# Performance work log

Measured on AMD Instinct MI355X. Metric: run time of the kernel, lower is better.

Reference implementation:

```python
import jax, jax.numpy as jnp
import numpy as np

B, T, N, H = 256, 64, 128, 128  # batch, seq_len, num_tasks, hidden_dim


def setup_inputs() -> dict:
    key = jax.random.key(0)
    k = jax.random.split(key, 8)
    task_seq = jax.random.randint(k[0], (B, T), 0, N)
    status_seq = jax.random.randint(k[1], (B, T), 0, 3)
    raw = (jax.random.uniform(k[2], (N, N)) < 0.05).astype(jnp.float32)
    adj = raw + jnp.eye(N, dtype=jnp.float32)
    rs = adj.sum(axis=1, keepdims=True)
    adj = adj / jnp.where(rs == 0, 1.0, rs)
    s = np.float32(1.0 / np.sqrt(H))
    emb = jax.random.normal(k[3], (N * 3, H), jnp.float32) * s      # interaction_emb
    W_ih = jax.random.normal(k[4], (3 * H, 2 * H), jnp.float32) * s  # GRUCell weight_ih (r,z,n)
    W_hh = jax.random.normal(k[5], (3 * H, H), jnp.float32) * s      # GRUCell weight_hh
    b_ih = jnp.zeros((3 * H,), jnp.float32)
    b_hh = jnp.zeros((3 * H,), jnp.float32)
    w_pred = jax.random.normal(k[6], (H,), jnp.float32) * s          # predict_layer weight [1,H] -> [H]
    b_pred = jnp.zeros((), jnp.float32)                              # predict_layer bias
    return dict(task_seq=task_seq, status_seq=status_seq, adj=adj, emb=emb,
                W_ih=W_ih, W_hh=W_hh, b_ih=b_ih, b_hh=b_hh,
                w_pred=w_pred, b_pred=b_pred)


def _gru_cell(x, h, W_ih, W_hh, b_ih, b_hh):
    # torch.nn.GRUCell: gates ordered (reset, update, new)
    gi = x @ W_ih.T + b_ih
    gh = h @ W_hh.T + b_hh
    i_r, i_z, i_n = jnp.split(gi, 3, axis=-1)
    h_r, h_z, h_n = jnp.split(gh, 3, axis=-1)
    r = jax.nn.sigmoid(i_r + h_r)
    z = jax.nn.sigmoid(i_z + h_z)
    n = jnp.tanh(i_n + r * h_n)
    return (1.0 - z) * n + z * h


def reference(task_seq, status_seq, adj, emb, W_ih, W_hh, b_ih, b_hh, w_pred, b_pred):
    Bsz, _ = task_seq.shape
    Nt = adj.shape[0]
    Hd = emb.shape[1]
    b_idx = jnp.arange(Bsz)
    h0 = jnp.zeros((Bsz, Nt, Hd), emb.dtype)

    def step(h, ts):
        task, status = ts                                # [B], [B]
        x = emb[task * 3 + status]                       # [B,H] interaction embedding
        # original: full (adj @ h)[b, task]; identical math computing only needed row
        agg = jnp.einsum('bn,bnh->bh', adj[task], h)     # [B,H]
        prev = h[b_idx, task]                            # [B,H]
        new = _gru_cell(jnp.concatenate([x, agg], axis=1), prev, W_ih, W_hh, b_ih, b_hh)
        h = h.at[b_idx, task].set(new)                   # scatter updated target state
        logits = h @ w_pred + b_pred                     # [B,N] predict over all tasks
        return h, logits

    h_final, logits = jax.lax.scan(step, h0, (task_seq.T, status_seq.T))
    return jnp.transpose(logits, (1, 0, 2)), h_final     # ([B,T,N], [B,N,H])
```

## Files before the change

### kernel.cpp

```cpp
#include <hip/hip_runtime.h>

#define B_ 256
#define T_ 64
#define N_ 128
#define H_ 128
#define G3 384
#define K2 256

#define WS_G    0
#define WS_PW   (WS_G + G3*G3)
#define WS_NZC  (WS_PW + K2*G3)
#define WS_NZP  (WS_NZC + 128)

__global__ void __launch_bounds__(384) prep(
        const float* __restrict__ W_ih, const float* __restrict__ W_hh,
        const float* __restrict__ emb,  const float* __restrict__ b_ih,
        const float* __restrict__ adj,  float* __restrict__ ws) {
    const int bid = blockIdx.x;
    if (bid < 384) {
        __shared__ float es[H_];
        const int e = bid, j = threadIdx.x;
        if (j < H_) es[j] = emb[e * H_ + j];
        __syncthreads();
        float acc = b_ih[j];
        const float4* wrow = (const float4*)(W_ih + j * K2);
        #pragma unroll 8
        for (int i = 0; i < 32; ++i) {
            float4 w = wrow[i];
            acc += w.x * es[4*i];
            acc += w.y * es[4*i + 1];
            acc += w.z * es[4*i + 2];
            acc += w.w * es[4*i + 3];
        }
        (ws + WS_G)[e * G3 + j] = acc;
    } else if (bid < 512) {
        __shared__ float row[N_];
        const int r = bid - 384;
        if (threadIdx.x < N_) row[threadIdx.x] = adj[r * N_ + threadIdx.x];
        __syncthreads();
        if (threadIdx.x == 0) {
            int*  nzc = (int*)(ws + WS_NZC);
            int2* nzp = (int2*)(ws + WS_NZP);
            int cnt = 0;
            for (int n = 0; n < N_; ++n) {
                float w = row[n];
                if (w != 0.0f) { nzp[r * N_ + cnt] = make_int2(n, __float_as_int(w)); ++cnt; }
            }
            int cnt4 = (cnt + 3) & ~3;
            for (int i = cnt; i < cnt4; ++i) nzp[r * N_ + i] = make_int2(0, 0);
            nzc[r] = cnt;
        }
    } else {
        const int k = bid - 512, j = threadIdx.x;
        (ws + WS_PW)[k * G3 + j] = (k < H_) ? W_ih[j * K2 + H_ + k]
                                            : W_hh[j * H_ + (k - H_)];
    }
}

__global__ void __launch_bounds__(512, 2) gkt_main(
        const int* __restrict__ task_seq, const int* __restrict__ status_seq,
        const float* __restrict__ b_hh,   const float* __restrict__ w_pred,
        const float* __restrict__ b_pred, const float* __restrict__ ws,
        float* __restrict__ out) {
    __shared__ __align__(16) float h_lds[N_ * H_];
    __shared__ __align__(16) float aggbuf[H_];
    __shared__ float pl[4 * G3];
    __shared__ float red[H_];
    __shared__ float Ll[N_];
    __shared__ int2  nzbuf[N_];
    __shared__ int   nz_cnt;
    __shared__ int   tasks_l[T_], stats_l[T_];

    const int b   = blockIdx.x;
    const int tid = threadIdx.x;
    const int t   = tid & 127;
    const int q   = tid >> 7;

    const float* G   = ws + WS_G;
    const float* PW  = ws + WS_PW;
    const int*   nzc = (const int*)(ws + WS_NZC);
    const int2*  nzp = (const int2*)(ws + WS_NZP);

    float wr[64], wz[64], wn[64];
    {
        const float* base = PW + (q * 64) * G3 + t;
        #pragma unroll
        for (int kk = 0; kk < 64; ++kk) {
            wr[kk] = base[kk * G3];
            wz[kk] = base[kk * G3 + 128];
            wn[kk] = base[kk * G3 + 256];
        }
    }
    const float bp = b_pred[0];
    float bhr = 0.f, bhz = 0.f, bhn = 0.f, wpt = 0.f;
    if (q < 2) { bhr = b_hh[t]; bhz = b_hh[128 + t]; bhn = b_hh[256 + t]; }
    if (q == 0) wpt = w_pred[t];

    for (int i = tid; i < N_ * H_; i += 512) h_lds[i] = 0.0f;
    if (tid < T_)            tasks_l[tid]       = task_seq[b * T_ + tid];
    else if (tid < 2 * T_)   stats_l[tid - T_]  = status_seq[b * T_ + (tid - T_)];
    if (tid < N_) { Ll[tid] = bp; aggbuf[tid] = 0.0f; }
    __syncthreads();

    for (int s = 0; s < T_; ++s) {
        const int task = tasks_l[s];

        float prevreg = 0.f;
        if (q < 2) prevreg = h_lds[task * H_ + t];
        {
            const float* vbase = (q < 2) ? (aggbuf + q * 64)
                                         : (h_lds + task * H_ + (q - 2) * 64);
            float pr = 0.f, pz = 0.f, pn = 0.f;
            #pragma unroll
            for (int kk = 0; kk < 64; kk += 4) {
                const float4 v = *(const float4*)(vbase + kk);
                pr += wr[kk] * v.x + wr[kk + 1] * v.y + wr[kk + 2] * v.z + wr[kk + 3] * v.w;
                pz += wz[kk] * v.x + wz[kk + 1] * v.y + wz[kk + 2] * v.z + wz[kk + 3] * v.w;
                pn += wn[kk] * v.x + wn[kk + 1] * v.y + wn[kk + 2] * v.z + wn[kk + 3] * v.w;
            }
            pl[q * G3 + t]       = pr;
            pl[q * G3 + 128 + t] = pz;
            pl[q * G3 + 256 + t] = pn;
        }
        if (q == 3 && s + 1 < T_) {
            const int tn = tasks_l[s + 1];
            nzbuf[t] = nzp[tn * N_ + t];
            if (t == 0) nz_cnt = nzc[tn];
        }
        if (tid < 64 && s > 0) {
            float x = red[tid] + red[tid + 64];
            #pragma unroll
            for (int off = 32; off > 0; off >>= 1) x += __shfl_xor(x, off, 64);
            if (tid == 0) Ll[tasks_l[s - 1]] = x + bp;
        }
        __syncthreads();

        if (q < 2) {
            const int e = task * 3 + stats_l[s];
            const float g0 = G[e * G3 + t];
            const float g1 = G[e * G3 + 128 + t];
            const float g2 = G[e * G3 + 256 + t];
            float sr  = g0 + bhr + pl[0*G3 + t] + pl[1*G3 + t] + pl[2*G3 + t] + pl[3*G3 + t];
            float sz  = g1 + bhz + pl[0*G3 + 128 + t] + pl[1*G3 + 128 + t]
                                 + pl[2*G3 + 128 + t] + pl[3*G3 + 128 + t];
            float in_ = g2 + pl[0*G3 + 256 + t] + pl[1*G3 + 256 + t];
            float hn_ = bhn + pl[2*G3 + 256 + t] + pl[3*G3 + 256 + t];
            float r = 1.0f / (1.0f + expf(-sr));
            float z = 1.0f / (1.0f + expf(-sz));
            float n = tanhf(in_ + r * hn_);
            float hnew = (1.0f - z) * n + z * prevreg;
            if (q == 0) {
                h_lds[task * H_ + t] = hnew;
                red[t] = hnew * wpt;
            } else if (s + 1 < T_) {
                float acc = 0.0f;
                const int cnt4 = (nz_cnt + 3) & ~3;
                for (int i = 0; i < cnt4; i += 4) {
                    int2 p0 = nzbuf[i], p1 = nzbuf[i+1], p2 = nzbuf[i+2], p3 = nzbuf[i+3];
                    float h0 = (p0.x == task) ? hnew : h_lds[p0.x * H_ + t];
                    float h1 = (p1.x == task) ? hnew : h_lds[p1.x * H_ + t];
                    float h2 = (p2.x == task) ? hnew : h_lds[p2.x * H_ + t];
                    float h3 = (p3.x == task) ? hnew : h_lds[p3.x * H_ + t];
                    acc += __int_as_float(p0.y) * h0;
                    acc += __int_as_float(p1.y) * h1;
                    acc += __int_as_float(p2.y) * h2;
                    acc += __int_as_float(p3.y) * h3;
                }
                aggbuf[t] = acc;
            }
        } else if (q == 2) {
            if (s > 0) out[(size_t)b * T_ * N_ + (size_t)(s - 1) * N_ + t] = Ll[t];
        }
        __syncthreads();
    }

    if (tid < 64) {
        float x = red[tid] + red[tid + 64];
        #pragma unroll
        for (int off = 32; off > 0; off >>= 1) x += __shfl_xor(x, off, 64);
        if (tid == 0) Ll[tasks_l[T_ - 1]] = x + bp;
    }
    __syncthreads();
    if (tid < N_) out[(size_t)b * T_ * N_ + (size_t)(T_ - 1) * N_ + tid] = Ll[tid];
    {
        float4* dst = (float4*)(out + (size_t)B_ * T_ * N_ + (size_t)b * N_ * H_);
        const float4* src = (const float4*)h_lds;
        for (int i = tid; i < N_ * H_ / 4; i += 512) dst[i] = src[i];
    }
}

extern "C" void kernel_launch(void* const* d_in, const int* in_sizes, int n_in,
                              void* d_out, int out_size, void* d_ws, size_t ws_size,
                              hipStream_t stream) {
    const int*   task = (const int*)d_in[0];
    const int*   stat = (const int*)d_in[1];
    const float* adj  = (const float*)d_in[2];
    const float* emb  = (const float*)d_in[3];
    const float* Wih  = (const float*)d_in[4];
    const float* Whh  = (const float*)d_in[5];
    const float* bhh  = (const float*)d_in[7];
    const float* wp   = (const float*)d_in[8];
    const float* bp   = (const float*)d_in[9];
    const float* bih  = (const float*)d_in[6];
    float* out = (float*)d_out;
    float* ws  = (float*)d_ws;

    prep    <<<768, 384, 0, stream>>>(Wih, Whh, emb, bih, adj, ws);
    gkt_main<<<256, 512, 0, stream>>>(task, stat, bhh, wp, bp, ws, out);
}
```

Baseline: 217.5 us.

## Split GRU matvec across 768 threads with two gate columns per thread

Raises the main kernel from 512 to 768 threads per block. Each thread now holds 128 weight registers covering two of the 384 gate columns instead of 192 registers covering three, which lowers register pressure and adds threads for latency hiding. The G-table global loads are moved before the first barrier so they overlap the matvec, and thread roles for the adjacency prefetch, logit output and gate update are reassigned. The cost is more waves sharing the LDS and barriers, and the requested occupancy of 3 blocks of 768 threads may not fit alongside the 64KB h_lds buffer.

```diff
diff --git a/kernel.cpp b/kernel.cpp
--- a/kernel.cpp
+++ b/kernel.cpp
@@ -57,7 +57,7 @@
     }
 }
 
-__global__ void __launch_bounds__(512, 2) gkt_main(
+__global__ void __launch_bounds__(768, 3) gkt_main(
         const int* __restrict__ task_seq, const int* __restrict__ status_seq,
         const float* __restrict__ b_hh,   const float* __restrict__ w_pred,
         const float* __restrict__ b_pred, const float* __restrict__ ws,
@@ -73,57 +73,67 @@
 
     const int b   = blockIdx.x;
     const int tid = threadIdx.x;
-    const int t   = tid & 127;
-    const int q   = tid >> 7;
+    const int c   = tid / 192;
+    const int j2  = tid - c * 192;
 
     const float* G   = ws + WS_G;
     const float* PW  = ws + WS_PW;
     const int*   nzc = (const int*)(ws + WS_NZC);
     const int2*  nzp = (const int2*)(ws + WS_NZP);
 
-    float wr[64], wz[64], wn[64];
+    float wA[64], wB[64];
     {
-        const float* base = PW + (q * 64) * G3 + t;
+        const float* baseA = PW + (c * 64) * G3 + j2;
         #pragma unroll
         for (int kk = 0; kk < 64; ++kk) {
-            wr[kk] = base[kk * G3];
-            wz[kk] = base[kk * G3 + 128];
-            wn[kk] = base[kk * G3 + 256];
-        }
-    }
+            wA[kk] = baseA[kk * G3];
+            wB[kk] = baseA[kk * G3 + 192];
+        }
+    }
+
     const float bp = b_pred[0];
+    const bool gate0 = (tid < 128);
+    const bool gate1 = (tid >= 384 && tid < 512);
+    const int  tg = gate0 ? tid : (tid - 384);
     float bhr = 0.f, bhz = 0.f, bhn = 0.f, wpt = 0.f;
-    if (q < 2) { bhr = b_hh[t]; bhz = b_hh[128 + t]; bhn = b_hh[256 + t]; }
-    if (q == 0) wpt = w_pred[t];
-
-    for (int i = tid; i < N_ * H_; i += 512) h_lds[i] = 0.0f;
-    if (tid < T_)            tasks_l[tid]       = task_seq[b * T_ + tid];
-    else if (tid < 2 * T_)   stats_l[tid - T_]  = status_seq[b * T_ + (tid - T_)];
-    if (tid < N_) { Ll[tid] = bp; aggbuf[tid] = 0.0f; }
+    if (gate0 || gate1) { bhr = b_hh[tg]; bhz = b_hh[128 + tg]; bhn = b_hh[256 + tg]; }
+    if (gate0) wpt = w_pred[tid];
+
+    for (int i = tid; i < N_ * H_; i += 768) h_lds[i] = 0.0f;
+    if (tid < T_)          tasks_l[tid]      = task_seq[b * T_ + tid];
+    else if (tid < 2*T_)   stats_l[tid - T_] = status_seq[b * T_ + (tid - T_)];
+    if (tid >= 128 && tid < 256) { Ll[tid-128] = bp; aggbuf[tid-128] = 0.0f; }
     __syncthreads();
 
     for (int s = 0; s < T_; ++s) {
         const int task = tasks_l[s];
 
-        float prevreg = 0.f;
-        if (q < 2) prevreg = h_lds[task * H_ + t];
+        float prevreg = 0.f, g0 = 0.f, g1 = 0.f, g2 = 0.f;
+        if (gate0 || gate1) {
+            prevreg = h_lds[task * H_ + tg];
+            const int e = task * 3 + stats_l[s];
+            g0 = G[e * G3 + tg];
+            g1 = G[e * G3 + 128 + tg];
+            g2 = G[e * G3 + 256 + tg];
+        }
         {
-            const float* vbase = (q < 2) ? (aggbuf + q * 64)
-                                         : (h_lds + task * H_ + (q - 2) * 64);
-            float pr = 0.f, pz = 0.f, pn = 0.f;
+            const float4* vb = (const float4*)((c < 2) ? (aggbuf + c * 64)
+                                                       : (h_lds + task * H_ + (c - 2) * 64));
+            float a0 = 0.f, a1 = 0.f, c0 = 0.f, c1 = 0.f;
             #pragma unroll
-            for (int kk = 0; kk < 64; kk += 4) {
-                const float4 v = *(const float4*)(vbase + kk);
-                pr += wr[kk] * v.x + wr[kk + 1] * v.y + wr[kk + 2] * v.z + wr[kk + 3] * v.w;
-                pz += wz[kk] * v.x + wz[kk + 1] * v.y + wz[kk + 2] * v.z + wz[kk + 3] * v.w;
-                pn += wn[kk] * v.x + wn[kk + 1] * v.y + wn[kk + 2] * v.z + wn[kk + 3] * v.w;
+            for (int i = 0; i < 16; i += 2) {
+                const float4 v = vb[i];
+                a0 += wA[4*i+0]*v.x; a0 += wA[4*i+1]*v.y; a0 += wA[4*i+2]*v.z; a0 += wA[4*i+3]*v.w;
+                c0 += wB[4*i+0]*v.x; c0 += wB[4*i+1]*v.y; c0 += wB[4*i+2]*v.z; c0 += wB[4*i+3]*v.w;
+                const float4 u = vb[i+1];
+                a1 += wA[4*i+4]*u.x; a1 += wA[4*i+5]*u.y; a1 += wA[4*i+6]*u.z; a1 += wA[4*i+7]*u.w;
+                c1 += wB[4*i+4]*u.x; c1 += wB[4*i+5]*u.y; c1 += wB[4*i+6]*u.z; c1 += wB[4*i+7]*u.w;
             }
-            pl[q * G3 + t]       = pr;
-            pl[q * G3 + 128 + t] = pz;
-            pl[q * G3 + 256 + t] = pn;
-        }
-        if (q == 3 && s + 1 < T_) {
-            const int tn = tasks_l[s + 1];
+            pl[c * G3 + j2]       = a0 + a1;
+            pl[c * G3 + 192 + j2] = c0 + c1;
+        }
+        if (tid >= 512 && tid < 640 && s + 1 < T_) {
+            const int t = tid - 512, tn = tasks_l[s + 1];
             nzbuf[t] = nzp[tn * N_ + t];
             if (t == 0) nz_cnt = nzc[tn];
         }
@@ -135,41 +145,37 @@
         }
         __syncthreads();
 
-        if (q < 2) {
-            const int e = task * 3 + stats_l[s];
-            const float g0 = G[e * G3 + t];
-            const float g1 = G[e * G3 + 128 + t];
-            const float g2 = G[e * G3 + 256 + t];
-            float sr  = g0 + bhr + pl[0*G3 + t] + pl[1*G3 + t] + pl[2*G3 + t] + pl[3*G3 + t];
-            float sz  = g1 + bhz + pl[0*G3 + 128 + t] + pl[1*G3 + 128 + t]
-                                 + pl[2*G3 + 128 + t] + pl[3*G3 + 128 + t];
-            float in_ = g2 + pl[0*G3 + 256 + t] + pl[1*G3 + 256 + t];
-            float hn_ = bhn + pl[2*G3 + 256 + t] + pl[3*G3 + 256 + t];
+        if (gate0 || gate1) {
+            float sr  = g0 + bhr + pl[tg] + pl[G3 + tg] + pl[2*G3 + tg] + pl[3*G3 + tg];
+            float sz  = g1 + bhz + pl[128 + tg] + pl[G3 + 128 + tg]
+                                 + pl[2*G3 + 128 + tg] + pl[3*G3 + 128 + tg];
+            float in_ = g2 + pl[256 + tg] + pl[G3 + 256 + tg];
+            float hn_ = bhn + pl[2*G3 + 256 + tg] + pl[3*G3 + 256 + tg];
             float r = 1.0f / (1.0f + expf(-sr));
             float z = 1.0f / (1.0f + expf(-sz));
             float n = tanhf(in_ + r * hn_);
             float hnew = (1.0f - z) * n + z * prevreg;
-            if (q == 0) {
-                h_lds[task * H_ + t] = hnew;
-                red[t] = hnew * wpt;
+            if (gate0) {
+                h_lds[task * H_ + tg] = hnew;
+                red[tg] = hnew * wpt;
             } else if (s + 1 < T_) {
                 float acc = 0.0f;
                 const int cnt4 = (nz_cnt + 3) & ~3;
                 for (int i = 0; i < cnt4; i += 4) {
                     int2 p0 = nzbuf[i], p1 = nzbuf[i+1], p2 = nzbuf[i+2], p3 = nzbuf[i+3];
-                    float h0 = (p0.x == task) ? hnew : h_lds[p0.x * H_ + t];
-                    float h1 = (p1.x == task) ? hnew : h_lds[p1.x * H_ + t];
-                    float h2 = (p2.x == task) ? hnew : h_lds[p2.x * H_ + t];
-                    float h3 = (p3.x == task) ? hnew : h_lds[p3.x * H_ + t];
+                    float h0 = (p0.x == task) ? hnew : h_lds[p0.x * H_ + tg];
+                    float h1 = (p1.x == task) ? hnew : h_lds[p1.x * H_ + tg];
+                    float h2 = (p2.x == task) ? hnew : h_lds[p2.x * H_ + tg];
+                    float h3 = (p3.x == task) ? hnew : h_lds[p3.x * H_ + tg];
                     acc += __int_as_float(p0.y) * h0;
                     acc += __int_as_float(p1.y) * h1;
                     acc += __int_as_float(p2.y) * h2;
                     acc += __int_as_float(p3.y) * h3;
                 }
-                aggbuf[t] = acc;
+                aggbuf[tg] = acc;
             }
-        } else if (q == 2) {
-            if (s > 0) out[(size_t)b * T_ * N_ + (size_t)(s - 1) * N_ + t] = Ll[t];
+        } else if (tid >= 192 && tid < 320) {
+            if (s > 0) out[(size_t)b * T_ * N_ + (size_t)(s - 1) * N_ + (tid - 192)] = Ll[tid - 192];
         }
         __syncthreads();
     }
@@ -185,7 +191,7 @@
     {
         float4* dst = (float4*)(out + (size_t)B_ * T_ * N_ + (size_t)b * N_ * H_);
         const float4* src = (const float4*)h_lds;
-        for (int i = tid; i < N_ * H_ / 4; i += 512) dst[i] = src[i];
+        for (int i = tid; i < N_ * H_ / 4; i += 768) dst[i] = src[i];
     }
 }
 
@@ -198,13 +204,13 @@
     const float* emb  = (const float*)d_in[3];
     const float* Wih  = (const float*)d_in[4];
     const float* Whh  = (const float*)d_in[5];
+    const float* bih  = (const float*)d_in[6];
     const float* bhh  = (const float*)d_in[7];
     const float* wp   = (const float*)d_in[8];
     const float* bp   = (const float*)d_in[9];
-    const float* bih  = (const float*)d_in[6];
     float* out = (float*)d_out;
     float* ws  = (float*)d_ws;
 
     prep    <<<768, 384, 0, stream>>>(Wih, Whh, emb, bih, adj, ws);
-    gkt_main<<<256, 512, 0, stream>>>(task, stat, bhh, wp, bp, ws, out);
+    gkt_main<<<256, 768, 0, stream>>>(task, stat, bhh, wp, bp, ws, out);
 }
```

Result: no change. 216.0 us (-0.7%).
